# Optimization experiments

Measured on AMD Instinct MI355X. Metric: run time of the kernel, lower is better.

Reference implementation:

```python
import jax
import jax.numpy as jnp
from jax import lax
import numpy as np

B, CIN, HIN, WIN = 4, 3, 128, 128
COUT, K, STRIDE = 64, 3, 2
NUM_NEIGHBORS = 7  # rank <= 6 keeps 7 nearest (incl. self), matching the torch code


def setup_inputs() -> dict:
    key = jax.random.key(0)
    kx, kw, kb = jax.random.split(key, 3)
    x = jax.random.normal(kx, (B, CIN, HIN, WIN), dtype=jnp.float32)
    w = jax.random.normal(kw, (COUT, CIN, K, K), dtype=jnp.float32) * 0.05
    b = jax.random.normal(kb, (COUT,), dtype=jnp.float32) * 0.05
    return {"x": x, "w": w, "b": b}


def reference(x, w, b):
    # head: Conv2d(in_feats, out_feats, kernel_size=3, stride=2, padding=1)
    pad = K // 2
    y4 = lax.conv_general_dilated(
        x, w, window_strides=(STRIDE, STRIDE),
        padding=((pad, pad), (pad, pad)),
        dimension_numbers=("NCHW", "OIHW", "NCHW"),
    ) + b[None, :, None, None]
    Bb, C, H, W = y4.shape
    N = H * W
    # [B, C, N] -> [B, N, C] node features
    y = jnp.transpose(y4.reshape(Bb, C, N), (0, 2, 1))

    # Adjacency built from detached features (original uses .detach().numpy())
    yd = lax.stop_gradient(y)
    sq = jnp.sum(yd * yd, axis=-1)  # [B, N]
    d2 = sq[:, :, None] + sq[:, None, :] - 2.0 * jnp.einsum("bnc,bmc->bnm", yd, yd)
    dist = jnp.sqrt(jnp.maximum(d2, 0.0))  # euclidean cdist, [B, N, N]
    # double argsort along axis=1 of each NxN matrix == rank within each row
    rank = jnp.argsort(jnp.argsort(dist, axis=2), axis=2)
    adj = jnp.where(rank <= NUM_NEIGHBORS - 1, 1.0, 0.0).astype(jnp.float32)
    return y, adj
```

## Files before the change

kernel.cpp:

```cpp
#include <hip/hip_runtime.h>
#include <stdint.h>

#define BATCH 4
#define CINCH 3
#define HIN 128
#define WIN 128
#define NN 4096
#define CF 64
#define KNN 7

typedef unsigned short u16;
typedef unsigned u32;
typedef unsigned long long u64;
typedef __attribute__((ext_vector_type(8))) short bf16x8;
typedef __attribute__((ext_vector_type(4))) float f32x4;

__device__ __forceinline__ u64 u64min(u64 a, u64 b) { return a < b ? a : b; }
__device__ __forceinline__ u32 u32min(u32 a, u32 b) { return a < b ? a : b; }

__device__ __forceinline__ u32 med3_u32(u32 a, u32 b, u32 c) {
    u32 d;
    asm("v_med3_u32 %0, %1, %2, %3" : "=v"(d) : "v"(a), "v"(b), "v"(c));
    return d;
}

__device__ __forceinline__ void insert8_med3(u32* l, u32 k) {
    l[7] = med3_u32(l[6], l[7], k);
    l[6] = med3_u32(l[5], l[6], k);
    l[5] = med3_u32(l[4], l[5], k);
    l[4] = med3_u32(l[3], l[4], k);
    l[3] = med3_u32(l[2], l[3], k);
    l[2] = med3_u32(l[1], l[2], k);
    l[1] = med3_u32(l[0], l[1], k);
    l[0] = u32min(l[0], k);
}

template <int M>
__device__ __forceinline__ void insertM64(u64* lst, u64 k) {
    u64 cur = k;
#pragma unroll
    for (int i = 0; i < M; ++i) {
        u64 lo = u64min(lst[i], cur);
        u64 hi = (lst[i] < cur) ? cur : lst[i];
        lst[i] = lo;
        cur = hi;
    }
}

__global__ __launch_bounds__(256) void conv_fused_kernel(
    const float* __restrict__ x, const float* __restrict__ w,
    const float* __restrict__ bias, float* __restrict__ y,
    u16* __restrict__ ybf, float* __restrict__ sq) {
    __shared__ float ws[CF * CINCH * 9];
    __shared__ float bs[CF];
    for (int i = threadIdx.x; i < CF * CINCH * 9; i += 256) ws[i] = w[i];
    if (threadIdx.x < CF) bs[threadIdx.x] = bias[threadIdx.x];
    __syncthreads();

    int gid = blockIdx.x * 256 + threadIdx.x;
    int c = gid & 63;
    int n = (gid >> 6) & (NN - 1);
    int b = gid >> 18;
    int oh = n >> 6, ow = n & 63;
    const float* xb = x + (size_t)b * CINCH * HIN * WIN;
    float acc = bs[c];
#pragma unroll
    for (int cin = 0; cin < CINCH; ++cin) {
#pragma unroll
        for (int kh = 0; kh < 3; ++kh) {
            int ih = oh * 2 - 1 + kh;
            if (ih < 0 || ih >= HIN) continue;
#pragma unroll
            for (int kw = 0; kw < 3; ++kw) {
                int iw = ow * 2 - 1 + kw;
                if (iw < 0 || iw >= WIN) continue;
                acc += xb[(cin * HIN + ih) * WIN + iw] *
                       ws[(c * CINCH + cin) * 9 + kh * 3 + kw];
            }
        }
    }
    y[(size_t)gid] = acc;

    uint32_t u = __float_as_uint(acc);
    u16 hv = (u16)((u + 0x7fffu + ((u >> 16) & 1u)) >> 16);
    size_t ti = ((size_t)(b * 256 + (n >> 4)) * 8 + (c >> 3)) * 128 +
                (size_t)(n & 15) * 8 + (c & 7);
    ybf[ti] = hv;

    float s = acc * acc;
#pragma unroll
    for (int off = 32; off; off >>= 1) s += __shfl_xor(s, off, 64);
    if (c == 0) sq[gid >> 6] = s;
}

__global__ __launch_bounds__(256, 4) void screen_kernel(
    const u16* __restrict__ ybf, const float* __restrict__ yf,
    const float* __restrict__ sq, float* __restrict__ adj) {
    __shared__ float sqlds[NN];
    __shared__ u32 mlds[16 * 129];
    __shared__ u64 ckey[16][32];
    __shared__ u32 cidx[16][32];

    const int bid = blockIdx.x;
    const int b = bid >> 8;
    const int r0 = (bid & 255) << 4;
    const int tid = threadIdx.x, w = tid >> 6, lane = tid & 63;
    const int lc = lane & 15, g = lane >> 4;
    const size_t nb = (size_t)b * NN;

    {
        const float4* s4 = (const float4*)(sq + nb);
        float4* d4 = (float4*)sqlds;
#pragma unroll
        for (int i = 0; i < 4; ++i) d4[i * 256 + tid] = s4[i * 256 + tid];
    }

    const size_t rb = ((size_t)(b * 256) + (r0 >> 4)) * 1024 + (size_t)lane * 8;
    bf16x8 rf0 = *(const bf16x8*)(ybf + rb);
    bf16x8 rf1 = *(const bf16x8*)(ybf + rb + 512);
    const float sqr = sq[nb + r0 + lc];

    u32 lst[8];
#pragma unroll
    for (int q = 0; q < 8; ++q) lst[q] = 0xFFFFFFFFu;

    const int c0 = w * 1024;
    const size_t tb = ((size_t)(b * 256) + (w << 6)) * 1024 + (size_t)lane * 8;

    f32x4* zrow = (f32x4*)(adj + (nb + r0 + (tid >> 4)) * NN) + (tid & 15);
    const f32x4 zf4 = {0.f, 0.f, 0.f, 0.f};

    bf16x8 slot[4][2];
#pragma unroll
    for (int j = 0; j < 4; ++j) {
        slot[j][0] = *(const bf16x8*)(ybf + tb + (size_t)j * 1024);
        slot[j][1] = *(const bf16x8*)(ybf + tb + (size_t)j * 1024 + 512);
    }

    __syncthreads();

    const f32x4 zro = {0.f, 0.f, 0.f, 0.f};

#define CONSUME(J, CT, REFILL)                                                  \
    {                                                                           \
        bf16x8 a0 = slot[J][0], a1 = slot[J][1];                                \
        if (REFILL) {                                                           \
            slot[J][0] = *(const bf16x8*)(ybf + tb + (size_t)((CT) + 4) * 1024);       \
            slot[J][1] = *(const bf16x8*)(ybf + tb + (size_t)((CT) + 4) * 1024 + 512); \
        }                                                                       \
        zrow[(CT) * 16] = zf4;     \
        f32x4 sc = *(const f32x4*)&sqlds[c0 + (CT) * 16 + g * 4];               \
        f32x4 acc = __builtin_amdgcn_mfma_f32_16x16x32_bf16(a0, rf0, zro, 0, 0, 0); \
        acc = __builtin_amdgcn_mfma_f32_16x16x32_bf16(a1, rf1, acc, 0, 0, 0);   \
        _Pragma("unroll")                                                       \
        for (int r = 0; r < 4; ++r) {                                           \
            float d2a = fmaxf((sqr + sc[r]) - 2.f * acc[r], 0.f);               \
            u32 key = (__float_as_uint(d2a) & 0xFFFFFF00u) | (u32)((CT) * 4 + r); \
            insert8_med3(lst, key);                                             \
        }                                                                       \
    }

    for (int g16 = 0; g16 < 15; ++g16) {
        const int ct0 = g16 * 4;
        CONSUME(0, ct0 + 0, 1)
        CONSUME(1, ct0 + 1, 1)
        CONSUME(2, ct0 + 2, 1)
        CONSUME(3, ct0 + 3, 1)
    }
    CONSUME(0, 60, 0)
    CONSUME(1, 61, 0)
    CONSUME(2, 62, 0)
    CONSUME(3, 63, 0)
#undef CONSUME

#pragma unroll
    for (int q = 0; q < 8; ++q)
        mlds[lc * 129 + (w * 4 + g) * 8 + q] = lst[q];
    __syncthreads();

    if (tid < 64) {
        const int mrow = tid >> 2, s4 = tid & 3;
        u64 top8[8];
#pragma unroll
        for (int q = 0; q < 8; ++q) top8[q] = ~0ull;
#pragma unroll
        for (int s = 0; s < 4; ++s) {
            const int src = s4 * 4 + s;
            const u32 colhi = (src >> 2) * 1024 + (src & 3) * 4;
#pragma unroll
            for (int q = 0; q < 8; ++q) {
                u32 k = mlds[mrow * 129 + src * 8 + q];
                u32 idx8 = k & 0xFFu;
                u32 col = colhi + (idx8 >> 2) * 16 + (idx8 & 3);
                u64 mk = ((u64)(k & 0xFFFFFF00u) << 24) | col;
                if (mk < top8[7]) insertM64<8>(top8, mk);
            }
        }
#pragma unroll
        for (int q = 0; q < 8; ++q)
            cidx[mrow][s4 * 8 + q] = (u32)(top8[q] & 0xFFFu);
    }
    __syncthreads();

    {
        const int rrow = tid >> 4, s = tid & 15;
        const float4* yr = (const float4*)(yf + (nb + r0 + rrow) * CF);
        const float sr = sqlds[r0 + rrow];
#pragma unroll
        for (int j2 = 0; j2 < 2; ++j2) {
            const int q = s * 2 + j2;
            const u32 col = cidx[rrow][q];
            const float4* yc = (const float4*)(yf + (nb + col) * CF);
            float a = 0.f;
#pragma unroll
            for (int k = 0; k < 16; ++k) {
                float4 av = yr[k], bv = yc[k];
                a += av.x * bv.x;
                a += av.y * bv.y;
                a += av.z * bv.z;
                a += av.w * bv.w;
            }
            float d2 = (sr + sqlds[col]) - 2.0f * a;
            float dd = sqrtf(fmaxf(d2, 0.0f));
            ckey[rrow][q] = ((u64)__float_as_uint(dd) << 32) | col;
        }
    }
    __syncthreads();

    if (tid < 16) {
        u64 t7[KNN];
#pragma unroll
        for (int q = 0; q < KNN; ++q) t7[q] = ~0ull;
#pragma unroll
        for (int q = 0; q < 32; ++q) {
            u64 k = ckey[tid][q];
            if (k < t7[KNN - 1]) insertM64<KNN>(t7, k);
        }
#pragma unroll
        for (int q = 0; q < KNN; ++q)
            cidx[tid][q] = (u32)(t7[q] & 0xFFFFFFFFu);
    }
    __syncthreads();

    if (tid < 16 * KNN) {
        const int orow = tid / KNN, q = tid % KNN;
        u32 col = cidx[orow][q];
        adj[(nb + r0 + orow) * NN + col] = 1.0f;
    }
}

extern "C" void kernel_launch(void* const* d_in, const int* in_sizes, int n_in,
                              void* d_out, int out_size, void* d_ws, size_t ws_size,
                              hipStream_t stream) {
    const float* x = (const float*)d_in[0];
    const float* w = (const float*)d_in[1];
    const float* bias = (const float*)d_in[2];

    float* y = (float*)d_out;
    float* adj = (float*)d_out + (size_t)BATCH * NN * CF;

    float* sq = (float*)d_ws;
    u16* ybf = (u16*)((char*)d_ws + 65536);

    conv_fused_kernel<<<4096, 256, 0, stream>>>(x, w, bias, y, ybf, sq);
    screen_kernel<<<1024, 256, 0, stream>>>(ybf, y, sq, adj);
}
```

Measured before the change: 95.93 us.

## Process 32 query rows per block to reuse column tiles across two row tiles

Measured after the change: 124.7 us. 30.0% more time.

```diff
diff --git a/kernel.cpp b/kernel.cpp
--- a/kernel.cpp
+++ b/kernel.cpp
@@ -96,67 +96,74 @@
 __global__ __launch_bounds__(256, 4) void screen_kernel(
     const u16* __restrict__ ybf, const float* __restrict__ yf,
     const float* __restrict__ sq, float* __restrict__ adj) {
-    __shared__ float sqlds[NN];
-    __shared__ u32 mlds[16 * 129];
-    __shared__ u64 ckey[16][32];
-    __shared__ u32 cidx[16][32];
+    __shared__ u32 mlds[32 * 129];
+    __shared__ u64 ckey[32][32];
+    __shared__ u32 cidx[32][32];
 
     const int bid = blockIdx.x;
-    const int b = bid >> 8;
-    const int r0 = (bid & 255) << 4;
+    const int b = bid >> 7;
+    const int r0 = (bid & 127) << 5;
+    const int rt = (bid & 127) * 2;
     const int tid = threadIdx.x, w = tid >> 6, lane = tid & 63;
     const int lc = lane & 15, g = lane >> 4;
     const size_t nb = (size_t)b * NN;
 
-    {
-        const float4* s4 = (const float4*)(sq + nb);
-        float4* d4 = (float4*)sqlds;
-#pragma unroll
-        for (int i = 0; i < 4; ++i) d4[i * 256 + tid] = s4[i * 256 + tid];
-    }
-
-    const size_t rb = ((size_t)(b * 256) + (r0 >> 4)) * 1024 + (size_t)lane * 8;
-    bf16x8 rf0 = *(const bf16x8*)(ybf + rb);
-    bf16x8 rf1 = *(const bf16x8*)(ybf + rb + 512);
-    const float sqr = sq[nb + r0 + lc];
-
-    u32 lst[8];
-#pragma unroll
-    for (int q = 0; q < 8; ++q) lst[q] = 0xFFFFFFFFu;
+    bf16x8 rf[2][2];
+    float sqr[2];
+#pragma unroll
+    for (int j = 0; j < 2; ++j) {
+        const size_t rbj = ((size_t)(b * 256) + rt + j) * 1024 + (size_t)lane * 8;
+        rf[j][0] = *(const bf16x8*)(ybf + rbj);
+        rf[j][1] = *(const bf16x8*)(ybf + rbj + 512);
+        sqr[j] = sq[nb + r0 + j * 16 + lc];
+    }
+
+    u32 lst[2][8];
+#pragma unroll
+    for (int j = 0; j < 2; ++j)
+#pragma unroll
+        for (int q = 0; q < 8; ++q) lst[j][q] = 0xFFFFFFFFu;
 
     const int c0 = w * 1024;
     const size_t tb = ((size_t)(b * 256) + (w << 6)) * 1024 + (size_t)lane * 8;
-
-    f32x4* zrow = (f32x4*)(adj + (nb + r0 + (tid >> 4)) * NN) + (tid & 15);
+    const float* scp = sq + nb + c0 + g * 4;
+
+    f32x4* zrowA = (f32x4*)(adj + (nb + r0 + (tid >> 4)) * NN) + (tid & 15);
+    f32x4* zrowB = (f32x4*)(adj + (nb + r0 + 16 + (tid >> 4)) * NN) + (tid & 15);
     const f32x4 zf4 = {0.f, 0.f, 0.f, 0.f};
 
     bf16x8 slot[4][2];
+    f32x4 scs[4];
 #pragma unroll
     for (int j = 0; j < 4; ++j) {
         slot[j][0] = *(const bf16x8*)(ybf + tb + (size_t)j * 1024);
         slot[j][1] = *(const bf16x8*)(ybf + tb + (size_t)j * 1024 + 512);
-    }
-
-    __syncthreads();
+        scs[j] = *(const f32x4*)(scp + j * 16);
+    }
 
     const f32x4 zro = {0.f, 0.f, 0.f, 0.f};
 
 #define CONSUME(J, CT, REFILL)                                                  \
     {                                                                           \
         bf16x8 a0 = slot[J][0], a1 = slot[J][1];                                \
+        f32x4 sc = scs[J];                                                      \
         if (REFILL) {                                                           \
             slot[J][0] = *(const bf16x8*)(ybf + tb + (size_t)((CT) + 4) * 1024);       \
             slot[J][1] = *(const bf16x8*)(ybf + tb + (size_t)((CT) + 4) * 1024 + 512); \
+            scs[J] = *(const f32x4*)(scp + ((CT) + 4) * 16);                    \
         }                                                                       \
-        zrow[(CT) * 16] = zf4;     \
-        f32x4 sc = *(const f32x4*)&sqlds[c0 + (CT) * 16 + g * 4];               \
-        f32x4 acc = __builtin_amdgcn_mfma_f32_16x16x32_bf16(a0, rf0, zro, 0, 0, 0); \
-        acc = __builtin_amdgcn_mfma_f32_16x16x32_bf16(a1, rf1, acc, 0, 0, 0);   \
+        zrowA[(CT) * 16] = zf4;                                                 \
+        zrowB[(CT) * 16] = zf4;                                                 \
         _Pragma("unroll")                                                       \
-        for (int r = 0; r < 4; ++r) {                                           \
-            float d2a = fmaxf((sqr + sc[r]) - 2.f * acc[r], 0.f);               \
-            u32 key = (__float_as_uint(d2a) & 0xFFFFFF00u) | (u32)((CT) * 4 + r); \
-            insert8_med3(lst, key);                                             \
+        for (int j = 0; j < 2; ++j) {                                           \
+            f32x4 acc = __builtin_amdgcn_mfma_f32_16x16x32_bf16(a0, rf[j][0], zro, 0, 0, 0); \
+            acc = __builtin_amdgcn_mfma_f32_16x16x32_bf16(a1, rf[j][1], acc, 0, 0, 0);       \
+            _Pragma("unroll")                                                   \
+            for (int r = 0; r < 4; ++r) {                                       \
+                float d2a = fmaxf((sqr[j] + sc[r]) - 2.f * acc[r], 0.f);        \
+                u32 key = (__float_as_uint(d2a) & 0xFFFFFF00u) | (u32)((CT) * 4 + r); \
+                insert8_med3(lst[j], key);                                      \
+            }                                                                   \
         }                                                                       \
     }
 
@@ -174,11 +181,13 @@
 #undef CONSUME
 
 #pragma unroll
-    for (int q = 0; q < 8; ++q)
-        mlds[lc * 129 + (w * 4 + g) * 8 + q] = lst[q];
-    __syncthreads();
-
-    if (tid < 64) {
+    for (int j = 0; j < 2; ++j)
+#pragma unroll
+        for (int q = 0; q < 8; ++q)
+            mlds[(j * 16 + lc) * 129 + (w * 4 + g) * 8 + q] = lst[j][q];
+    __syncthreads();
+
+    if (tid < 128) {
         const int mrow = tid >> 2, s4 = tid & 3;
         u64 top8[8];
 #pragma unroll
@@ -203,12 +212,12 @@
     __syncthreads();
 
     {
-        const int rrow = tid >> 4, s = tid & 15;
+        const int rrow = tid >> 3, s = tid & 7;
         const float4* yr = (const float4*)(yf + (nb + r0 + rrow) * CF);
-        const float sr = sqlds[r0 + rrow];
-#pragma unroll
-        for (int j2 = 0; j2 < 2; ++j2) {
-            const int q = s * 2 + j2;
+        const float sr = sq[nb + r0 + rrow];
+#pragma unroll
+        for (int j2 = 0; j2 < 4; ++j2) {
+            const int q = s * 4 + j2;
             const u32 col = cidx[rrow][q];
             const float4* yc = (const float4*)(yf + (nb + col) * CF);
             float a = 0.f;
@@ -220,14 +229,14 @@
                 a += av.z * bv.z;
                 a += av.w * bv.w;
             }
-            float d2 = (sr + sqlds[col]) - 2.0f * a;
+            float d2 = (sr + sq[nb + col]) - 2.0f * a;
             float dd = sqrtf(fmaxf(d2, 0.0f));
             ckey[rrow][q] = ((u64)__float_as_uint(dd) << 32) | col;
         }
     }
     __syncthreads();
 
-    if (tid < 16) {
+    if (tid < 32) {
         u64 t7[KNN];
 #pragma unroll
         for (int q = 0; q < KNN; ++q) t7[q] = ~0ull;
@@ -242,7 +251,7 @@
     }
     __syncthreads();
 
-    if (tid < 16 * KNN) {
+    if (tid < 32 * KNN) {
         const int orow = tid / KNN, q = tid % KNN;
         u32 col = cidx[orow][q];
         adj[(nb + r0 + orow) * NN + col] = 1.0f;
@@ -263,5 +272,5 @@
     u16* ybf = (u16*)((char*)d_ws + 65536);
 
     conv_fused_kernel<<<4096, 256, 0, stream>>>(x, w, bias, y, ybf, sq);
-    screen_kernel<<<1024, 256, 0, stream>>>(ybf, y, sq, adj);
-}
+    screen_kernel<<<512, 256, 0, stream>>>(ybf, y, sq, adj);
+}
```
